# Kernel optimization log

Measured on AMD Instinct MI355X. Metric: run time of the kernel, lower is better.

## Reference

```python
import jax, jax.numpy as jnp
import numpy as np

D_MODEL, N_HEAD, D_FF = 768, 12, 3072
HEAD_DIM = D_MODEL // N_HEAD
EPS = 1e-5


def _layernorm(x, g, b):
    mu = jnp.mean(x, axis=-1, keepdims=True)
    var = jnp.mean((x - mu) ** 2, axis=-1, keepdims=True)
    return (x - mu) * jax.lax.rsqrt(var + EPS) * g + b


def setup_inputs() -> dict:
    key = jax.random.key(0)
    ks = jax.random.split(key, 14)
    s = 1.0 / np.sqrt(D_MODEL)
    sf = 1.0 / np.sqrt(D_FF)
    inp = {
        "x": jax.random.normal(ks[0], (2, 2048, D_MODEL), dtype=jnp.float32),
        "Wq": jax.random.normal(ks[1], (D_MODEL, D_MODEL), dtype=jnp.float32) * s,
        "bq": jnp.zeros((D_MODEL,), jnp.float32),
        "Wk": jax.random.normal(ks[2], (D_MODEL, D_MODEL), dtype=jnp.float32) * s,
        "bk": jnp.zeros((D_MODEL,), jnp.float32),
        "Wv": jax.random.normal(ks[3], (D_MODEL, D_MODEL), dtype=jnp.float32) * s,
        "bv": jnp.zeros((D_MODEL,), jnp.float32),
        "Wo": jax.random.normal(ks[4], (D_MODEL, D_MODEL), dtype=jnp.float32) * s,
        "bo": jnp.zeros((D_MODEL,), jnp.float32),
        "W1": jax.random.normal(ks[5], (D_MODEL, D_FF), dtype=jnp.float32) * s,
        "b1": jnp.zeros((D_FF,), jnp.float32),
        "W2": jax.random.normal(ks[6], (D_FF, D_MODEL), dtype=jnp.float32) * sf,
        "b2": jnp.zeros((D_MODEL,), jnp.float32),
        "ln1_g": jnp.ones((D_MODEL,), jnp.float32),
        "ln1_b": jnp.zeros((D_MODEL,), jnp.float32),
        "ln2_g": jnp.ones((D_MODEL,), jnp.float32),
        "ln2_b": jnp.zeros((D_MODEL,), jnp.float32),
    }
    return inp


def reference(x, Wq, bq, Wk, bk, Wv, bv, Wo, bo, W1, b1, W2, b2,
              ln1_g, ln1_b, ln2_g, ln2_b):
    B, S, D = x.shape
    # projections -> [B, H, S, hd]
    def proj(W, b):
        return (x @ W + b).reshape(B, S, N_HEAD, HEAD_DIM).transpose(0, 2, 1, 3)
    q, k, v = proj(Wq, bq), proj(Wk, bk), proj(Wv, bv)
    scores = jnp.einsum("bhqd,bhkd->bhqk", q, k) / jnp.sqrt(
        jnp.asarray(HEAD_DIM, jnp.float32))
    attn = jax.nn.softmax(scores, axis=-1)
    ctx = jnp.einsum("bhqk,bhkd->bhqd", attn, v)
    ctx = ctx.transpose(0, 2, 1, 3).reshape(B, S, D)
    attn_out = ctx @ Wo + bo
    h = _layernorm(x + attn_out, ln1_g, ln1_b)
    ffn = jax.nn.gelu(h @ W1 + b1, approximate=False) @ W2 + b2
    return _layernorm(h + ffn, ln2_g, ln2_b)
```

## Files before the change

kernel.cpp:

```cpp
#include <hip/hip_runtime.h>
#include <hip/hip_bf16.h>
#include <cstdint>
#include <cstddef>

typedef unsigned short u16;
typedef __bf16 bf16x8 __attribute__((ext_vector_type(8)));
typedef float f32x4 __attribute__((ext_vector_type(4)));

#define MFMA_BF16(a, b, c) __builtin_amdgcn_mfma_f32_16x16x32_bf16((a), (b), (c), 0, 0, 0)

#define GLDS16(g, l)                                                        \
  __builtin_amdgcn_global_load_lds(                                         \
      (__attribute__((address_space(1))) void*)(void*)(g),                  \
      (__attribute__((address_space(3))) void*)(void*)(l), 16, 0, 0)

#define QSCALE 0.18033688011112042f
#define PSTRIDE ((size_t)4096 * 768)

__device__ __forceinline__ u16 f2bf(float x) {
  union { float f; unsigned u; } c; c.f = x;
  unsigned u = c.u;
  unsigned r = (u + 0x7fffu + ((u >> 16) & 1u)) >> 16;
  return (u16)r;
}


__global__ __launch_bounds__(256) void transpose4_k(
    const float* __restrict__ s0, const float* __restrict__ s1,
    const float* __restrict__ s2, const float* __restrict__ s3,
    u16* __restrict__ d0, u16* __restrict__ d1,
    u16* __restrict__ d2, u16* __restrict__ d3) {
  __shared__ float tile[32][33];
  const float* in; u16* out;
  switch (blockIdx.z) {
    case 0: in = s0; out = d0; break;
    case 1: in = s1; out = d1; break;
    case 2: in = s2; out = d2; break;
    default: in = s3; out = d3; break;
  }
  const int tx = threadIdx.x & 31, ty = threadIdx.x >> 5;
  const int bx = blockIdx.x * 32, by = blockIdx.y * 32;
#pragma unroll
  for (int j = 0; j < 32; j += 8)
    tile[ty + j][tx] = in[(size_t)(by + ty + j) * 768 + bx + tx];
  __syncthreads();
#pragma unroll
  for (int j = 0; j < 32; j += 8)
    out[(size_t)(bx + ty + j) * 768 + by + tx] = f2bf(tile[tx][ty + j]);
}

__global__ __launch_bounds__(256) void transpose_bf16_k(
    const float* __restrict__ in, u16* __restrict__ out, int K, int N) {
  __shared__ float tile[32][33];
  const int tx = threadIdx.x & 31, ty = threadIdx.x >> 5;
  const int bx = blockIdx.x * 32, by = blockIdx.y * 32;
#pragma unroll
  for (int j = 0; j < 32; j += 8)
    tile[ty + j][tx] = in[(size_t)(by + ty + j) * N + bx + tx];
  __syncthreads();
#pragma unroll
  for (int j = 0; j < 32; j += 8)
    out[(size_t)(bx + ty + j) * K + by + tx] = f2bf(tile[tx][ty + j]);
}

__global__ __launch_bounds__(256) void cvt_bf16_k(
    const float* __restrict__ in, u16* __restrict__ out, int n) {
  int i = (blockIdx.x * 256 + threadIdx.x) * 4;
  if (i + 3 < n) {
    const float4 v = *(const float4*)(in + i);
    ushort4 o;
    o.x = f2bf(v.x); o.y = f2bf(v.y); o.z = f2bf(v.z); o.w = f2bf(v.w);
    *(ushort4*)(out + i) = o;
  }
}

__global__ __launch_bounds__(256) void concat3_k(
    const float* __restrict__ a, const float* __restrict__ b,
    const float* __restrict__ c, float* __restrict__ out) {
  int i = blockIdx.x * 256 + threadIdx.x;
  if (i < 768) out[i] = a[i];
  else if (i < 1536) out[i] = b[i - 768];
  else if (i < 2304) out[i] = c[i - 1536];
}

template <int EPI>
__global__ __launch_bounds__(256) void gemm_bt(
    const u16* __restrict__ A, const u16* __restrict__ BT,
    const float* __restrict__ bias, int M, int N, int K, int kchunk,
    float* __restrict__ outf, u16* __restrict__ outb,
    u16* __restrict__ qo, u16* __restrict__ ko, u16* __restrict__ vto) {
  __shared__ __align__(16) u16 lsA[2 * 128 * 32];
  __shared__ __align__(16) u16 lsB[2 * 128 * 32];
  const int tid = threadIdx.x;
  const int w = tid >> 6, lane = tid & 63;
  const int wm = w & 1, wn = w >> 1;
  const int lrow = lane & 15, quad = lane >> 4;
  const int m0 = blockIdx.y * 128, n0 = blockIdx.x * 128;
  const int kbeg = blockIdx.z * kchunk;

  f32x4 acc[4][4];
#pragma unroll
  for (int i = 0; i < 4; ++i)
#pragma unroll
    for (int j = 0; j < 4; ++j) acc[i][j] = (f32x4){0.f, 0.f, 0.f, 0.f};

  const int off = tid * 16;
  const int srow = off >> 6;
  const int schunk = (off >> 4) & 3;
  const int sxc = schunk ^ (srow & 3);
  const int scol = sxc * 8;

  const u16* ga0 = A + (size_t)(m0 + srow) * K + scol;
  const u16* gb0 = BT + (size_t)(n0 + srow) * K + scol;

  auto stage = [&](int k0, int buf) {
    char* da = (char*)(lsA + buf * 4096);
    char* db = (char*)(lsB + buf * 4096);
    GLDS16(ga0 + k0, da + off);
    GLDS16(ga0 + k0 + (size_t)64 * K, da + 4096 + off);
    GLDS16(gb0 + k0, db + off);
    GLDS16(gb0 + k0 + (size_t)64 * K, db + 4096 + off);
  };

  const int rs = (quad ^ (lrow & 3)) * 8;

  const int niter = kchunk >> 5;
  stage(kbeg, 0);
  for (int t = 0; t < niter; ++t) {
    __syncthreads();
    if (t + 1 < niter) stage(kbeg + (t + 1) * 32, (t + 1) & 1);
    const u16* Ab = lsA + (t & 1) * 4096;
    const u16* Bb = lsB + (t & 1) * 4096;
    bf16x8 af[4], bfr[4];
#pragma unroll
    for (int ms = 0; ms < 4; ++ms)
      af[ms] = *(const bf16x8*)&Ab[(wm * 64 + ms * 16 + lrow) * 32 + rs];
#pragma unroll
    for (int ns = 0; ns < 4; ++ns)
      bfr[ns] = *(const bf16x8*)&Bb[(wn * 64 + ns * 16 + lrow) * 32 + rs];
#pragma unroll
    for (int ms = 0; ms < 4; ++ms)
#pragma unroll
      for (int ns = 0; ns < 4; ++ns)
        acc[ms][ns] = MFMA_BF16(af[ms], bfr[ns], acc[ms][ns]);
  }

  float* const pf = (EPI == 3) ? outf + (size_t)blockIdx.z * M * N : outf;
#pragma unroll
  for (int ms = 0; ms < 4; ++ms) {
    const int rbase = m0 + wm * 64 + ms * 16 + quad * 4;
#pragma unroll
    for (int ns = 0; ns < 4; ++ns) {
      const int col = n0 + wn * 64 + ns * 16 + lrow;
      if constexpr (EPI == 3) {
#pragma unroll
        for (int r = 0; r < 4; ++r)
          pf[(size_t)(rbase + r) * N + col] = acc[ms][ns][r];
      } else if constexpr (EPI == 2) {
        const float bcol = bias[col];
#pragma unroll
        for (int r = 0; r < 4; ++r) {
          float v = acc[ms][ns][r] + bcol;
          float g = 0.5f * v * (1.0f + erff(v * 0.7071067811865476f));
          outb[(size_t)(rbase + r) * N + col] = f2bf(g);
        }
      } else {
        const float bcol = bias[col];
        const int which = col / 768;
        const int rem = col - which * 768;
        const int hh = rem >> 6, dd = rem & 63;
        const int bI = rbase >> 11, sI = rbase & 2047;
        const size_t bh = (size_t)bI * 12 + hh;
        if (which == 0) {
#pragma unroll
          for (int r = 0; r < 4; ++r)
            qo[(bh * 2048 + sI + r) * 64 + dd] = f2bf((acc[ms][ns][r] + bcol) * QSCALE);
        } else if (which == 1) {
#pragma unroll
          for (int r = 0; r < 4; ++r)
            ko[(bh * 2048 + sI + r) * 64 + dd] = f2bf(acc[ms][ns][r] + bcol);
        } else {
          ushort4 pk;
          pk.x = f2bf(acc[ms][ns][0] + bcol);
          pk.y = f2bf(acc[ms][ns][1] + bcol);
          pk.z = f2bf(acc[ms][ns][2] + bcol);
          pk.w = f2bf(acc[ms][ns][3] + bcol);
          *(ushort4*)(vto + (bh * 64 + dd) * 2048 + sI) = pk;
        }
      }
    }
  }
}

__global__ __launch_bounds__(256) void attn_kernel(
    const u16* __restrict__ q, const u16* __restrict__ k,
    const u16* __restrict__ vT, u16* __restrict__ opart,
    float* __restrict__ lpart) {
  __shared__ __align__(16) u16 lsK[2 * 64 * 64];
  __shared__ __align__(16) u16 lsV[2 * 64 * 64];
  __shared__ __align__(16) u16 lsP[4][32 * 64];
  const int tid = threadIdx.x;
  const int w = tid >> 6, lane = tid & 63;
  const int lrow = lane & 15, quad = lane >> 4;
  const int bh = blockIdx.y;
  const int b = bh / 12, h = bh - b * 12;
  const int q0 = blockIdx.x * 128;
  const int z = blockIdx.z;
  const int kvbeg = z * 1024;

  const u16* qbase = q + (size_t)bh * 2048 * 64;
  const u16* kbase = k + (size_t)bh * 2048 * 64;
  const u16* vbase = vT + (size_t)bh * 64 * 2048;

  bf16x8 qf[2][2];
#pragma unroll
  for (int m = 0; m < 2; ++m) {
    const int qrow = q0 + w * 32 + m * 16 + lrow;
    qf[m][0] = *(const bf16x8*)(qbase + (size_t)qrow * 64 + quad * 8);
    qf[m][1] = *(const bf16x8*)(qbase + (size_t)qrow * 64 + 32 + quad * 8);
  }

  float lsum[2][4] = {{0.f, 0.f, 0.f, 0.f}, {0.f, 0.f, 0.f, 0.f}};
  f32x4 oacc[2][4];
#pragma unroll
  for (int m = 0; m < 2; ++m)
#pragma unroll
    for (int d = 0; d < 4; ++d) oacc[m][d] = (f32x4){0.f, 0.f, 0.f, 0.f};

  const int off = tid * 16;
  const int srow = off >> 7;
  const int schunk = (off >> 4) & 7;
  const int sxc = schunk ^ (srow & 7);
  const int ksrc = srow * 64 + sxc * 8;
  const int vsrc0 = srow * 2048 + sxc * 8;

  const int c0 = quad ^ (lrow & 7);
  const int rd0 = c0 * 8, rd1 = (c0 ^ 4) * 8;

  u16* const lsPw = &lsP[w][0];
  const int jhi_base = lrow >> 3, jlo = lrow & 7;

  auto stage = [&](int kt, int buf) {
    char* dk = (char*)(lsK + buf * 4096);
    char* dv = (char*)(lsV + buf * 4096);
    GLDS16(kbase + (size_t)kt * 64 + ksrc, dk + off);
    GLDS16(kbase + (size_t)(kt + 32) * 64 + ksrc, dk + 4096 + off);
    GLDS16(vbase + vsrc0 + kt, dv + off);
    GLDS16(vbase + vsrc0 + kt + 32 * 2048, dv + 4096 + off);
  };

  stage(kvbeg, 0);
  for (int t = 0; t < 16; ++t) {
    __syncthreads();
    if (t < 15) stage(kvbeg + (t + 1) * 64, (t + 1) & 1);
    const u16* Kb = lsK + (t & 1) * 4096;
    const u16* Vb = lsV + (t & 1) * 4096;

    f32x4 sc[2][4];
#pragma unroll
    for (int ns = 0; ns < 4; ++ns) {
      const u16* kr = Kb + (ns * 16 + lrow) * 64;
      bf16x8 kf0 = *(const bf16x8*)(kr + rd0);
      bf16x8 kf1 = *(const bf16x8*)(kr + rd1);
#pragma unroll
      for (int m = 0; m < 2; ++m) {
        sc[m][ns] = (f32x4){0.f, 0.f, 0.f, 0.f};
        sc[m][ns] = MFMA_BF16(qf[m][0], kf0, sc[m][ns]);
        sc[m][ns] = MFMA_BF16(qf[m][1], kf1, sc[m][ns]);
      }
    }

#pragma unroll
    for (int m = 0; m < 2; ++m)
#pragma unroll
      for (int ns = 0; ns < 4; ++ns) {
        const int jhi = ns * 2 + jhi_base;
#pragma unroll
        for (int r = 0; r < 4; ++r) {
          float p = __builtin_amdgcn_exp2f(sc[m][ns][r]);
          lsum[m][r] += p;
          union { float f; unsigned u; } cv; cv.f = p;
          const int row7 = (quad * 4 + r) & 7;
          lsPw[(m * 16 + quad * 4 + r) * 64 + ((jhi ^ row7) * 8) + jlo] =
              (u16)(cv.u >> 16);
        }
      }

#pragma unroll
    for (int d = 0; d < 4; ++d) {
      const u16* vr = Vb + (d * 16 + lrow) * 64;
      bf16x8 vf0 = *(const bf16x8*)(vr + rd0);
      bf16x8 vf1 = *(const bf16x8*)(vr + rd1);
#pragma unroll
      for (int m = 0; m < 2; ++m) {
        const u16* pr = lsPw + (m * 16 + lrow) * 64;
        bf16x8 pf0 = *(const bf16x8*)(pr + rd0);
        bf16x8 pf1 = *(const bf16x8*)(pr + rd1);
        oacc[m][d] = MFMA_BF16(pf0, vf0, oacc[m][d]);
        oacc[m][d] = MFMA_BF16(pf1, vf1, oacc[m][d]);
      }
    }
  }

#pragma unroll
  for (int m = 0; m < 2; ++m)
#pragma unroll
    for (int r = 0; r < 4; ++r) {
#pragma unroll
      for (int mm = 1; mm <= 8; mm <<= 1)
        lsum[m][r] += __shfl_xor(lsum[m][r], mm);
    }

  u16* const op = opart + (size_t)z * PSTRIDE;
#pragma unroll
  for (int m = 0; m < 2; ++m) {
    const int srow_out = q0 + w * 32 + m * 16 + quad * 4;
#pragma unroll
    for (int d = 0; d < 4; ++d)
#pragma unroll
      for (int r = 0; r < 4; ++r)
        op[(size_t)(b * 2048 + srow_out + r) * 768 + h * 64 + d * 16 + lrow] =
            f2bf(oacc[m][d][r]);
    if (lrow == 0) {
#pragma unroll
      for (int r = 0; r < 4; ++r)
        lpart[(size_t)(z * 24 + bh) * 2048 + srow_out + r] = lsum[m][r];
    }
  }
}

__global__ __launch_bounds__(256) void attn_combine_k(
    const u16* __restrict__ op, const float* __restrict__ lp,
    u16* __restrict__ ctx) {
  const unsigned idx = (blockIdx.x * 256u + threadIdx.x) * 4u;
  const unsigned row = idx / 768u;
  const unsigned c = idx - row * 768u;
  const int b = row >> 11, s = row & 2047;
  const int h = c >> 6;
  const size_t li = (size_t)(b * 12 + h) * 2048 + s;
  const float rinv = 1.f / (lp[li] + lp[(size_t)24 * 2048 + li]);
  ushort4 o0 = *(const ushort4*)(op + idx);
  ushort4 o1 = *(const ushort4*)(op + PSTRIDE + idx);
  ushort4 out;
  union { unsigned u; float f; } a, bb2;
#define CMB(fld) \
  a.u = (unsigned)o0.fld << 16; bb2.u = (unsigned)o1.fld << 16; \
  out.fld = f2bf((a.f + bb2.f) * rinv);
  CMB(x) CMB(y) CMB(z) CMB(w)
#undef CMB
  *(ushort4*)(ctx + idx) = out;
}

__global__ __launch_bounds__(256) void ln_kernel(
    const float* __restrict__ parts, int nparts, const float* __restrict__ bias,
    const float* __restrict__ res, const float* __restrict__ g,
    const float* __restrict__ bb, float* __restrict__ outf, u16* __restrict__ outb) {
  const int row = blockIdx.x;
  const int tid = threadIdx.x;
  const float* pr = res + (size_t)row * 768;
  float v[3], s = 0.f, s2 = 0.f;
#pragma unroll
  for (int j = 0; j < 3; ++j) {
    const int c = tid + j * 256;
    float t = bias[c] + pr[c];
    for (int p = 0; p < nparts; ++p)
      t += parts[p * PSTRIDE + (size_t)row * 768 + c];
    v[j] = t; s += t; s2 += t * t;
  }
#pragma unroll
  for (int m = 32; m > 0; m >>= 1) {
    s += __shfl_xor(s, m);
    s2 += __shfl_xor(s2, m);
  }
  __shared__ float red[8];
  const int w = tid >> 6, lane = tid & 63;
  if (lane == 0) { red[w] = s; red[4 + w] = s2; }
  __syncthreads();
  s = red[0] + red[1] + red[2] + red[3];
  s2 = red[4] + red[5] + red[6] + red[7];
  const float mu = s * (1.f / 768.f);
  const float var = s2 * (1.f / 768.f) - mu * mu;
  const float rstd = rsqrtf(var + 1e-5f);
#pragma unroll
  for (int j = 0; j < 3; ++j) {
    const int c = tid + j * 256;
    const float y = (v[j] - mu) * rstd * g[c] + bb[c];
    if (outf) outf[(size_t)row * 768 + c] = y;
    if (outb) outb[(size_t)row * 768 + c] = f2bf(y);
  }
}

extern "C" void kernel_launch(void* const* d_in, const int* in_sizes, int n_in,
                              void* d_out, int out_size, void* d_ws, size_t ws_size,
                              hipStream_t stream) {
  const float* x    = (const float*)d_in[0];
  const float* Wq   = (const float*)d_in[1];
  const float* bq   = (const float*)d_in[2];
  const float* Wk   = (const float*)d_in[3];
  const float* bk   = (const float*)d_in[4];
  const float* Wv   = (const float*)d_in[5];
  const float* bv   = (const float*)d_in[6];
  const float* Wo   = (const float*)d_in[7];
  const float* bo   = (const float*)d_in[8];
  const float* W1   = (const float*)d_in[9];
  const float* b1   = (const float*)d_in[10];
  const float* W2   = (const float*)d_in[11];
  const float* b2   = (const float*)d_in[12];
  const float* ln1g = (const float*)d_in[13];
  const float* ln1b = (const float*)d_in[14];
  const float* ln2g = (const float*)d_in[15];
  const float* ln2b = (const float*)d_in[16];

  char* ws = (char*)d_ws;
  size_t off = 0;
  auto alloc = [&](size_t bytes) {
    void* p = ws + off;
    off += (bytes + 255) & ~(size_t)255;
    return p;
  };
  u16*  WqkvT = (u16*)alloc(2304ull * 768 * 2);
  u16*  WoT   = (u16*)alloc(768ull * 768 * 2);
  u16*  W1T   = (u16*)alloc(3072ull * 768 * 2);
  u16*  W2T   = (u16*)alloc(768ull * 3072 * 2);
  float* bqkv = (float*)alloc(2304 * 4);
  char* bigbase = (char*)alloc(0);
  u16*  xb    = (u16*)alloc(4096ull * 768 * 2);
  u16*  qb    = (u16*)alloc(24ull * 2048 * 64 * 2);
  u16*  kb    = (u16*)alloc(24ull * 2048 * 64 * 2);
  u16*  vtb   = (u16*)alloc(24ull * 64 * 2048 * 2);
  u16*  ctx   = (u16*)alloc(4096ull * 768 * 2);
  float* attno = (float*)alloc(2ull * PSTRIDE * 4);
  float* f2b   = (float*)bigbase;
  u16*   opart = (u16*)attno;
  float* lpart = (float*)((char*)attno + 2 * PSTRIDE * 2);
  float* hbuf  = (float*)alloc(4096ull * 768 * 4);
  u16*  hb    = (u16*)alloc(4096ull * 768 * 2);
  u16*  f1    = (u16*)alloc(4096ull * 3072 * 2);

  transpose4_k<<<dim3(24, 24, 4), 256, 0, stream>>>(
      Wq, Wk, Wv, Wo, WqkvT, WqkvT + 768 * 768, WqkvT + 2 * 768 * 768, WoT);
  transpose_bf16_k<<<dim3(96, 24), 256, 0, stream>>>(W1, W1T, 768, 3072);
  transpose_bf16_k<<<dim3(24, 96), 256, 0, stream>>>(W2, W2T, 3072, 768);
  concat3_k<<<9, 256, 0, stream>>>(bq, bk, bv, bqkv);
  cvt_bf16_k<<<3072, 256, 0, stream>>>(x, xb, 4096 * 768);

  gemm_bt<0><<<dim3(18, 32, 1), 256, 0, stream>>>(xb, WqkvT, bqkv, 4096, 2304, 768, 768,
                                                  nullptr, nullptr, qb, kb, vtb);
  attn_kernel<<<dim3(16, 24, 2), 256, 0, stream>>>(qb, kb, vtb, opart, lpart);
  attn_combine_k<<<3072, 256, 0, stream>>>(opart, lpart, ctx);
  gemm_bt<3><<<dim3(6, 32, 2), 256, 0, stream>>>(ctx, WoT, nullptr, 4096, 768, 768, 384,
                                                 attno, nullptr, nullptr, nullptr, nullptr);
  ln_kernel<<<4096, 256, 0, stream>>>(attno, 2, bo, x, ln1g, ln1b, hbuf, hb);
  gemm_bt<2><<<dim3(24, 32, 1), 256, 0, stream>>>(hb, W1T, b1, 4096, 3072, 768, 768,
                                                  nullptr, f1, nullptr, nullptr, nullptr);
  gemm_bt<3><<<dim3(6, 32, 4), 256, 0, stream>>>(f1, W2T, nullptr, 4096, 768, 3072, 768,
                                                 f2b, nullptr, nullptr, nullptr, nullptr);
  ln_kernel<<<4096, 256, 0, stream>>>(f2b, 4, b2, hbuf, ln2g, ln2b, (float*)d_out, nullptr);
}
```

Baseline: 311.3 us.

## Fuse weight prep kernels and widen LDS XOR swizzle in GEMM tiles

Merges the four weight transpose/convert and bias concat launches into a single kernel that dispatches on block index, removing launch overhead. Changes the GEMM shared-memory tile layout to pack two 32-element rows per 128-byte line with an 8-way XOR swizzle, aiming to reduce LDS bank conflicts on the fragment reads. The swizzle mapping must stay consistent between the global-to-LDS stores and the MFMA fragment loads.

```diff
diff --git a/kernel.cpp b/kernel.cpp
--- a/kernel.cpp
+++ b/kernel.cpp
@@ -24,36 +24,40 @@
   return (u16)r;
 }
 
-
-__global__ __launch_bounds__(256) void transpose4_k(
-    const float* __restrict__ s0, const float* __restrict__ s1,
-    const float* __restrict__ s2, const float* __restrict__ s3,
-    u16* __restrict__ d0, u16* __restrict__ d1,
-    u16* __restrict__ d2, u16* __restrict__ d3) {
-  __shared__ float tile[32][33];
-  const float* in; u16* out;
-  switch (blockIdx.z) {
-    case 0: in = s0; out = d0; break;
-    case 1: in = s1; out = d1; break;
-    case 2: in = s2; out = d2; break;
-    default: in = s3; out = d3; break;
-  }
-  const int tx = threadIdx.x & 31, ty = threadIdx.x >> 5;
-  const int bx = blockIdx.x * 32, by = blockIdx.y * 32;
-#pragma unroll
-  for (int j = 0; j < 32; j += 8)
-    tile[ty + j][tx] = in[(size_t)(by + ty + j) * 768 + bx + tx];
-  __syncthreads();
-#pragma unroll
-  for (int j = 0; j < 32; j += 8)
-    out[(size_t)(bx + ty + j) * 768 + by + tx] = f2bf(tile[tx][ty + j]);
-}
-
-__global__ __launch_bounds__(256) void transpose_bf16_k(
-    const float* __restrict__ in, u16* __restrict__ out, int K, int N) {
+__global__ __launch_bounds__(256) void prep_weights_k(
+    const float* __restrict__ Wq, const float* __restrict__ Wk,
+    const float* __restrict__ Wv, const float* __restrict__ Wo,
+    const float* __restrict__ W1, const float* __restrict__ W2,
+    const float* __restrict__ bq, const float* __restrict__ bk,
+    const float* __restrict__ bv,
+    u16* __restrict__ WqkvT, u16* __restrict__ WoT,
+    u16* __restrict__ W1T, u16* __restrict__ W2T, float* __restrict__ bqkv) {
+  const int id = blockIdx.x;
+  if (id >= 6912) {
+    int i = (id - 6912) * 256 + threadIdx.x;
+    if (i < 768) bqkv[i] = bq[i];
+    else if (i < 1536) bqkv[i] = bk[i - 768];
+    else if (i < 2304) bqkv[i] = bv[i - 1536];
+    return;
+  }
+  const float* in; u16* out; int K, N, bx, by;
+  if (id < 2304) {
+    const int mat = id / 576, t = id - mat * 576;
+    in = (mat == 0) ? Wq : (mat == 1) ? Wk : (mat == 2) ? Wv : Wo;
+    out = (mat == 0) ? WqkvT : (mat == 1) ? WqkvT + 768 * 768
+        : (mat == 2) ? WqkvT + 2 * 768 * 768 : WoT;
+    K = 768; N = 768; bx = (t % 24) * 32; by = (t / 24) * 32;
+  } else if (id < 4608) {
+    const int t = id - 2304;
+    in = W1; out = W1T; K = 768; N = 3072;
+    bx = (t % 96) * 32; by = (t / 96) * 32;
+  } else {
+    const int t = id - 4608;
+    in = W2; out = W2T; K = 3072; N = 768;
+    bx = (t % 24) * 32; by = (t / 24) * 32;
+  }
   __shared__ float tile[32][33];
   const int tx = threadIdx.x & 31, ty = threadIdx.x >> 5;
-  const int bx = blockIdx.x * 32, by = blockIdx.y * 32;
 #pragma unroll
   for (int j = 0; j < 32; j += 8)
     tile[ty + j][tx] = in[(size_t)(by + ty + j) * N + bx + tx];
@@ -72,15 +76,6 @@
     o.x = f2bf(v.x); o.y = f2bf(v.y); o.z = f2bf(v.z); o.w = f2bf(v.w);
     *(ushort4*)(out + i) = o;
   }
-}
-
-__global__ __launch_bounds__(256) void concat3_k(
-    const float* __restrict__ a, const float* __restrict__ b,
-    const float* __restrict__ c, float* __restrict__ out) {
-  int i = blockIdx.x * 256 + threadIdx.x;
-  if (i < 768) out[i] = a[i];
-  else if (i < 1536) out[i] = b[i - 768];
-  else if (i < 2304) out[i] = c[i - 1536];
 }
 
 template <int EPI>
@@ -105,10 +100,11 @@
     for (int j = 0; j < 4; ++j) acc[i][j] = (f32x4){0.f, 0.f, 0.f, 0.f};
 
   const int off = tid * 16;
-  const int srow = off >> 6;
-  const int schunk = (off >> 4) & 3;
-  const int sxc = schunk ^ (srow & 3);
-  const int scol = sxc * 8;
+  const int line = tid >> 3;
+  const int slotp = tid & 7;
+  const int p = slotp ^ (line & 7);
+  const int srow = line * 2 + (p >> 2);
+  const int scol = (p & 3) * 8;
 
   const u16* ga0 = A + (size_t)(m0 + srow) * K + scol;
   const u16* gb0 = BT + (size_t)(n0 + srow) * K + scol;
@@ -122,7 +118,9 @@
     GLDS16(gb0 + k0 + (size_t)64 * K, db + 4096 + off);
   };
 
-  const int rs = (quad ^ (lrow & 3)) * 8;
+  const int lline = lrow >> 1;
+  const int lslot = (((lrow & 1) << 2) + quad) ^ ((lrow >> 1) & 7);
+  const int rdoff = lslot * 8;
 
   const int niter = kchunk >> 5;
   stage(kbeg, 0);
@@ -134,10 +132,10 @@
     bf16x8 af[4], bfr[4];
 #pragma unroll
     for (int ms = 0; ms < 4; ++ms)
-      af[ms] = *(const bf16x8*)&Ab[(wm * 64 + ms * 16 + lrow) * 32 + rs];
+      af[ms] = *(const bf16x8*)&Ab[(wm * 32 + ms * 8 + lline) * 64 + rdoff];
 #pragma unroll
     for (int ns = 0; ns < 4; ++ns)
-      bfr[ns] = *(const bf16x8*)&Bb[(wn * 64 + ns * 16 + lrow) * 32 + rs];
+      bfr[ns] = *(const bf16x8*)&Bb[(wn * 32 + ns * 8 + lline) * 64 + rdoff];
 #pragma unroll
     for (int ms = 0; ms < 4; ++ms)
 #pragma unroll
@@ -437,11 +435,8 @@
   u16*  hb    = (u16*)alloc(4096ull * 768 * 2);
   u16*  f1    = (u16*)alloc(4096ull * 3072 * 2);
 
-  transpose4_k<<<dim3(24, 24, 4), 256, 0, stream>>>(
-      Wq, Wk, Wv, Wo, WqkvT, WqkvT + 768 * 768, WqkvT + 2 * 768 * 768, WoT);
-  transpose_bf16_k<<<dim3(96, 24), 256, 0, stream>>>(W1, W1T, 768, 3072);
-  transpose_bf16_k<<<dim3(24, 96), 256, 0, stream>>>(W2, W2T, 3072, 768);
-  concat3_k<<<9, 256, 0, stream>>>(bq, bk, bv, bqkv);
+  prep_weights_k<<<6921, 256, 0, stream>>>(Wq, Wk, Wv, Wo, W1, W2, bq, bk, bv,
+                                           WqkvT, WoT, W1T, W2T, bqkv);
   cvt_bf16_k<<<3072, 256, 0, stream>>>(x, xb, 4096 * 768);
 
   gemm_bt<0><<<dim3(18, 32, 1), 256, 0, stream>>>(xb, WqkvT, bqkv, 4096, 2304, 768, 768,
```

Result: no change. 306.9 us (-1.4%).
